# Kernel optimization log

Hardware: AMD Instinct MI355X
Metric: run time of the kernel (lower is better)

Reference implementation:

```python
import math
import jax, jax.numpy as jnp
import numpy as np

NH, HD, CHUNK, PAST, FUT = 12, 128, 128, 127, 0  # heads, head_dim, chunk, left-1, right
CTX = CHUNK + PAST + FUT                          # 255
Q_SCALE = HD ** (-0.5) / math.log(2.0)
K_SCALE = math.log1p(math.e) / math.log(2.0)
SOFTCAP = 50.0


def setup_inputs() -> dict:
    key = jax.random.key(0)
    ks = jax.random.split(key, 8)
    B, S, H = 4, 4096, NH * HD
    return {
        "hidden_states": jax.random.normal(ks[0], (B, S, H), jnp.float32),
        "position_embeddings": jax.random.normal(ks[1], (CTX, H), jnp.float32),
        "Wq": jax.random.normal(ks[2], (H, H), jnp.float32) * 0.02,
        "Wk": jax.random.normal(ks[3], (H, H), jnp.float32) * 0.02,
        "Wv": jax.random.normal(ks[4], (H, H), jnp.float32) * 0.02,
        "Wrel": jax.random.normal(ks[5], (H, H), jnp.float32) * 0.02,
        "Wpost": jax.random.normal(ks[6], (H, H), jnp.float32) * 0.02,
        "per_dim_scale": jax.random.normal(ks[7], (HD,), jnp.float32) * 0.1,
    }


def reference(hidden_states, position_embeddings, Wq, Wk, Wv, Wrel, Wpost, per_dim_scale):
    B, S, H = hidden_states.shape
    # projections -> [B, S, nh, hd]; per-dim softplus scaling on queries (Gemma audio)
    q = (hidden_states @ Wq.T).reshape(B, S, NH, HD)
    q = q * (Q_SCALE * jax.nn.softplus(per_dim_scale))
    k = (hidden_states @ Wk.T).reshape(B, S, NH, HD) * K_SCALE
    v = (hidden_states @ Wv.T).reshape(B, S, NH, HD)

    NB = (S + CHUNK - 1) // CHUNK
    pad = NB * CHUNK - S
    q_blk = jnp.pad(q, ((0, 0), (0, pad), (0, 0), (0, 0))).reshape(B, NB, CHUNK, NH, HD)

    def extract_block_context(x):
        # pad [PAST] front, [FUT + CHUNK - 1] back; overlapping windows of CTX, stride CHUNK
        xp = jnp.pad(x, ((0, 0), (PAST, FUT + CHUNK - 1), (0, 0), (0, 0)))
        idx = jnp.arange(NB)[:, None] * CHUNK + jnp.arange(CTX)[None, :]  # [NB, CTX]
        return xp[:, idx]  # [B, NB, CTX, nh, hd]

    k_ctx = extract_block_context(k)
    v_ctx = extract_block_context(v)

    # content scores: [B, nh, NB, CHUNK, CTX]
    ac = jnp.einsum('bnchd,bnxhd->bhncx', q_blk, k_ctx)

    # relative-position scores with Transformer-XL style rel_shift
    rel_k = (position_embeddings @ Wrel.T).reshape(-1, NH, HD)  # [P, nh, hd]
    bd = jnp.einsum('bnchd,phd->bhncp', q_blk, rel_k)            # [B, nh, NB, CHUNK, P]
    P = bd.shape[-1]
    bd = jnp.pad(bd, ((0, 0), (0, 0), (0, 0), (0, 0), (0, CTX + 1 - P)))
    bd = bd.reshape(B, NH, NB, CHUNK * (CTX + 1))[..., : CHUNK * CTX]
    bd = bd.reshape(B, NH, NB, CHUNK, CTX)

    logits = SOFTCAP * jnp.tanh((ac + bd) / SOFTCAP)  # softcap
    w = jax.nn.softmax(logits, axis=-1)

    out = jnp.einsum('bhncx,bnxhd->bnchd', w, v_ctx)  # [B, NB, CHUNK, nh, hd]
    out = out.reshape(B, NB * CHUNK, NH * HD)[:, :S]
    return out @ Wpost.T
```

## Files before the change

### kernel.cpp

```cpp
#include <hip/hip_runtime.h>
#include <hip/hip_bf16.h>
#include <math.h>


#define NH_    12
#define HD_    128
#define H_     1536
#define B_     4
#define S_     4096
#define CHUNK_ 128
#define CTX_   255
#define NB_CH  32
#define QKW_   3072
#define BSTR_  4352

typedef unsigned short u16;
typedef short bf16x8 __attribute__((ext_vector_type(8)));
typedef float f32x4 __attribute__((ext_vector_type(4)));

static constexpr float Q_SCALE_F = (float)(0.08838834764831845 / 0.6931471805599453);
static constexpr float K_SCALE_F = (float)(1.3132616875182228 / 0.6931471805599453);

__device__ __forceinline__ u16 f2bf(float f) {
    __hip_bfloat16 h = __float2bfloat16(f);
    return __builtin_bit_cast(u16, h);
}
__device__ __forceinline__ float bf2f(u16 u) {
    unsigned int t = ((unsigned int)u) << 16;
    return __builtin_bit_cast(float, t);
}
__device__ __forceinline__ float fast_tanh(float t) {
    float u = __expf(-2.f * fabsf(t));
    float r = (1.f - u) / (1.f + u);
    return (t < 0.f) ? -r : r;
}

__device__ __forceinline__ void gload_lds16(const u16* src_global, u16* dst_lds) {
    __builtin_amdgcn_global_load_lds(
        (const __attribute__((address_space(1))) unsigned int*)src_global,
        (__attribute__((address_space(3))) unsigned int*)dst_lds,
        16, 0, 0);
}

__global__ __launch_bounds__(256)
void conv_bf16(const float* __restrict__ src, long long base,
               u16* __restrict__ dst, long long n,
               long long zero_below, long long zero_from,
               int mode, const float* __restrict__ pds, int ncols)
{
    long long i = ((long long)blockIdx.x * 256 + threadIdx.x) * 4;
    if (i >= n) return;
    float4 v = make_float4(0.f, 0.f, 0.f, 0.f);
    if (i >= zero_below && i < zero_from)
        v = *(const float4*)(src + base + i);
    float s = 1.f;
    if (mode == 1) {
        int row = (int)(i / ncols);
        float x = pds[row & 127];
        float sp = (x > 20.f) ? x : log1pf(__expf(x));
        s = Q_SCALE_F * sp;
    } else if (mode == 2) {
        s = K_SCALE_F;
    }
    ushort4 o = make_ushort4(f2bf(v.x * s), f2bf(v.y * s), f2bf(v.z * s), f2bf(v.w * s));
    *(ushort4*)(dst + i) = o;
}

__global__ __launch_bounds__(256)
void conv_hs(const float* __restrict__ src, long long src_row0,
             u16* __restrict__ dst, long long nelem)
{
    long long i = ((long long)blockIdx.x * 256 + threadIdx.x) * 4;
    if (i >= nelem) return;
    const int row = (int)(i / H_);
    const int col = (int)(i - (long long)row * H_);
    const int b = row / BSTR_;
    const int local = row - b * BSTR_;
    float4 v = make_float4(0.f, 0.f, 0.f, 0.f);
    if (local >= 128 && local < 128 + S_) {
        const long long srow = src_row0 + (long long)b * S_ + local - 128;
        v = *(const float4*)(src + srow * H_ + col);
    }
    ushort4 o = make_ushort4(f2bf(v.x), f2bf(v.y), f2bf(v.z), f2bf(v.w));
    *(ushort4*)(dst + i) = o;
}

#define STAGE(kt, bufc) do {                                                   \
    const int _ko = (kt) << 5;                                                 \
    gload_lds16(srcA[0] + _ko, lds + (bufc) * 4096 + pbase[0]);                \
    gload_lds16(srcA[1] + _ko, lds + (bufc) * 4096 + pbase[1]);                \
    gload_lds16(srcB[0] + _ko, lds + 16384 + (bufc) * 4096 + pbase[0]);        \
    gload_lds16(srcB[1] + _ko, lds + 16384 + (bufc) * 4096 + pbase[1]);        \
} while (0)

#define READF(afX, bfX, b) do {                                                \
    _Pragma("unroll")                                                          \
    for (int m = 0; m < 4; ++m)                                                \
        afX[m] = *(const bf16x8*)&lds[(b) * 4096 + (wr + m * 16 + lr) * 32 + sw8]; \
    _Pragma("unroll")                                                          \
    for (int n = 0; n < 4; ++n)                                                \
        bfX[n] = *(const bf16x8*)&lds[16384 + (b) * 4096 + (wc + n * 16 + lr) * 32 + sw8]; \
} while (0)

#define MFMA16(afX, bfX) do {                                                  \
    __builtin_amdgcn_s_setprio(1);                                             \
    _Pragma("unroll")                                                          \
    for (int m = 0; m < 4; ++m)                                                \
        _Pragma("unroll")                                                      \
        for (int n = 0; n < 4; ++n)                                            \
            acc[m][n] = __builtin_amdgcn_mfma_f32_16x16x32_bf16(afX[m], bfX[n], acc[m][n], 0, 0, 0); \
    __builtin_amdgcn_s_setprio(0);                                             \
} while (0)

#define ITER(t, b, afC, bfC, afN, bfN) do {                                    \
    if ((t) + 2 < nk) {                                                        \
        STAGE((t) + 2, ((b) + 2) & 3);                                         \
        asm volatile("s_waitcnt vmcnt(4)" ::: "memory");                       \
    } else {                                                                   \
        asm volatile("s_waitcnt vmcnt(0)" ::: "memory");                       \
    }                                                                          \
    __builtin_amdgcn_s_barrier();                                              \
    if ((t) + 1 < nk) READF(afN, bfN, ((b) + 1) & 3);                          \
    MFMA16(afC, bfC);                                                          \
} while (0)

template<int OUTB>
__global__ __launch_bounds__(256)
void gemm_bt(const u16* __restrict__ A, const u16* __restrict__ B,
             void* __restrict__ Cp, int M, int N, int K, int ldc)
{
    __shared__ __align__(16) u16 lds[32768];

    const int tid = threadIdx.x;
    const int w = tid >> 6, l = tid & 63;
    const int lr = l & 15, lg = l >> 4;
    const int bm = blockIdx.y * 128, bn = blockIdx.x * 128;
    const int wr = (w >> 1) * 64, wc = (w & 1) * 64;

    const int sw8 = (lg ^ ((lr >> 1) & 3)) * 8;

    const u16* srcA[2];
    const u16* srcB[2];
    int pbase[2];
#pragma unroll
    for (int c = 0; c < 2; ++c) {
        const int p = (w * 2 + c) * 64 + l;
        const int row = p >> 2;
        const int s_log = (p & 3) ^ ((row >> 1) & 3);
        pbase[c] = p * 8;
        srcA[c] = A + (size_t)(bm + row) * K + s_log * 8;
        srcB[c] = B + (size_t)(bn + row) * K + s_log * 8;
    }

    f32x4 acc[4][4];
#pragma unroll
    for (int m = 0; m < 4; ++m)
#pragma unroll
        for (int n = 0; n < 4; ++n) acc[m][n] = (f32x4){0.f, 0.f, 0.f, 0.f};

    const int nk = K >> 5;
    bf16x8 af0[4], bf0[4], af1[4], bf1[4];

    STAGE(0, 0);
    STAGE(1, 1);
    asm volatile("s_waitcnt vmcnt(4)" ::: "memory");
    __builtin_amdgcn_s_barrier();
    READF(af0, bf0, 0);

    for (int t0 = 0; t0 < nk; t0 += 4) {
        ITER(t0 + 0, 0, af0, bf0, af1, bf1);
        ITER(t0 + 1, 1, af1, bf1, af0, bf0);
        ITER(t0 + 2, 2, af0, bf0, af1, bf1);
        ITER(t0 + 3, 3, af1, bf1, af0, bf0);
    }

    if (OUTB) {
#pragma unroll
        for (int h = 0; h < 2; ++h) {
            if (wr == h * 64) {
#pragma unroll
                for (int m = 0; m < 4; ++m)
#pragma unroll
                    for (int n = 0; n < 4; ++n)
#pragma unroll
                        for (int r = 0; r < 4; ++r)
                            lds[(m * 16 + lg * 4 + r) * 136 + wc + n * 16 + lr] =
                                f2bf(acc[m][n][r]);
            }
            __syncthreads();
#pragma unroll
            for (int it = 0; it < 4; ++it) {
                const int sid = it * 256 + tid;
                const int row = sid >> 4, sl = sid & 15;
                int4 val = *(const int4*)&lds[row * 136 + sl * 8];
                *(int4*)((u16*)Cp + (size_t)(bm + h * 64 + row) * ldc + bn + sl * 8) = val;
            }
            __syncthreads();
        }
    } else {
#pragma unroll
        for (int m = 0; m < 4; ++m)
#pragma unroll
            for (int n = 0; n < 4; ++n)
#pragma unroll
                for (int r = 0; r < 4; ++r) {
                    const int row = bm + wr + m * 16 + lg * 4 + r;
                    const int col = bn + wc + n * 16 + lr;
                    ((float*)Cp)[(size_t)row * ldc + col] = acc[m][n][r];
                }
    }
}

__global__ __launch_bounds__(512)
void attn_mfma(const u16* __restrict__ qk, const u16* __restrict__ vT,
               const u16* __restrict__ relk, u16* __restrict__ attn_out,
               int vld)
{
    __shared__ __align__(16) u16 kv_s[256 * 128];
    __shared__ __align__(16) u16 g_s[128 * 264];

    const int ln = blockIdx.x, h = blockIdx.y, bz = blockIdx.z;
    const int tid = threadIdx.x;
    const int w = tid >> 6, l = tid & 63;
    const int lr = l & 15, lg = l >> 4;
    const size_t qbase = (size_t)bz * BSTR_;
    const size_t qrow0 = qbase + (size_t)(ln + 1) * 128;

    bf16x8 qa[4];
    {
        const u16* qp = qk + (qrow0 + w * 16 + lr) * QKW_ + h * HD_ + lg * 8;
#pragma unroll
        for (int kk = 0; kk < 4; ++kk) qa[kk] = *(const bf16x8*)(qp + kk * 32);
    }

#pragma unroll
    for (int it = 0; it < 8; ++it) {
        const int p = it * 512 + tid;
        const int row = p >> 4;
        const int s_log = (p & 15) ^ (row & 15);
        gload_lds16(relk + (size_t)row * H_ + h * HD_ + s_log * 8, kv_s + p * 8);
    }
    __syncthreads();

    f32x4 sacc[16];
#pragma unroll
    for (int n = 0; n < 16; ++n) sacc[n] = (f32x4){0.f, 0.f, 0.f, 0.f};
#pragma unroll
    for (int n = 0; n < 16; ++n)
#pragma unroll
        for (int kk = 0; kk < 4; ++kk) {
            int row = n * 16 + lr;
            int sl = kk * 4 + lg;
            bf16x8 bfrag = *(const bf16x8*)&kv_s[row * 128 + ((sl ^ (row & 15)) << 3)];
            sacc[n] = __builtin_amdgcn_mfma_f32_16x16x32_bf16(qa[kk], bfrag, sacc[n], 0, 0, 0);
        }

    const int c = w * 16 + lg * 4;
#pragma unroll
    for (int n = 0; n < 16; ++n)
#pragma unroll
        for (int r = 0; r < 4; ++r)
            g_s[(c + r) * 264 + n * 16 + lr] = f2bf(sacc[n][r]);
    __syncthreads();

#pragma unroll
    for (int it = 0; it < 8; ++it) {
        const int p = it * 512 + tid;
        const int row = p >> 4;
        const int s_log = (p & 15) ^ (row & 15);
        gload_lds16(qk + (qbase + (size_t)(ln * 128 + 1 + row)) * QKW_ + 1536 + h * HD_ + s_log * 8,
                    kv_s + p * 8);
    }
    __syncthreads();

#pragma unroll
    for (int n = 0; n < 16; ++n) sacc[n] = (f32x4){0.f, 0.f, 0.f, 0.f};
#pragma unroll
    for (int n = 0; n < 16; ++n)
#pragma unroll
        for (int kk = 0; kk < 4; ++kk) {
            int row = n * 16 + lr;
            int sl = kk * 4 + lg;
            bf16x8 bfrag = *(const bf16x8*)&kv_s[row * 128 + ((sl ^ (row & 15)) << 3)];
            sacc[n] = __builtin_amdgcn_mfma_f32_16x16x32_bf16(qa[kk], bfrag, sacc[n], 0, 0, 0);
        }

#pragma unroll
    for (int n = 0; n < 16; ++n)
#pragma unroll
        for (int r = 0; r < 4; ++r) {
            int cc = c + r;
            int x = n * 16 + lr;
            float val;
            if (x == 255) {
                val = -1e30f;
            } else {
                int dx = x - cc;
                u16 bdu = (dx >= 0) ? g_s[cc * 264 + dx]
                                    : g_s[(cc - 1) * 264 + dx + 256];
                float t = (sacc[n][r] + bf2f(bdu)) * (1.f / 50.f);
                val = 50.f * fast_tanh(t);
            }
            sacc[n][r] = val;
        }

#pragma unroll
    for (int r = 0; r < 4; ++r) {
        float m = -1e30f;
#pragma unroll
        for (int n = 0; n < 16; ++n) m = fmaxf(m, sacc[n][r]);
#pragma unroll
        for (int off = 1; off < 16; off <<= 1) m = fmaxf(m, __shfl_xor(m, off, 16));
        float s = 0.f;
#pragma unroll
        for (int n = 0; n < 16; ++n) {
            float e = __expf(sacc[n][r] - m);
            sacc[n][r] = e;
            s += e;
        }
#pragma unroll
        for (int off = 1; off < 16; off <<= 1) s += __shfl_xor(s, off, 16);
        float inv = 1.f / s;
#pragma unroll
        for (int n = 0; n < 16; ++n) sacc[n][r] *= inv;
    }
    __syncthreads();

#pragma unroll
    for (int n = 0; n < 16; ++n)
#pragma unroll
        for (int r = 0; r < 4; ++r)
            g_s[(c + r) * 264 + n * 16 + lr] = f2bf(sacc[n][r]);

#pragma unroll
    for (int it = 0; it < 8; ++it) {
        const int p = it * 512 + tid;
        const int d = p >> 5;
        const int s_log = (p & 31) ^ (d & 15);
        gload_lds16(vT + (size_t)(h * HD_ + d) * vld + qbase + ln * 128 + 1 + s_log * 8,
                    kv_s + p * 8);
    }
    __syncthreads();

    f32x4 oacc[8];
#pragma unroll
    for (int n = 0; n < 8; ++n) oacc[n] = (f32x4){0.f, 0.f, 0.f, 0.f};
#pragma unroll
    for (int kk = 0; kk < 8; ++kk) {
        int prow = w * 16 + lr;
        bf16x8 pa = *(const bf16x8*)&g_s[prow * 264 + kk * 32 + lg * 8];
#pragma unroll
        for (int n = 0; n < 8; ++n) {
            int d = n * 16 + lr;
            int sl = kk * 4 + lg;
            bf16x8 vb = *(const bf16x8*)&kv_s[d * 256 + ((sl ^ (d & 15)) << 3)];
            oacc[n] = __builtin_amdgcn_mfma_f32_16x16x32_bf16(pa, vb, oacc[n], 0, 0, 0);
        }
    }

    __syncthreads();
#pragma unroll
    for (int n = 0; n < 8; ++n)
#pragma unroll
        for (int r = 0; r < 4; ++r)
            kv_s[(c + r) * 136 + n * 16 + lr] = f2bf(oacc[n][r]);
    __syncthreads();
#pragma unroll
    for (int it = 0; it < 4; ++it) {
        const int sid = it * 512 + tid;
        const int row = sid >> 4, sl = sid & 15;
        int4 val = *(const int4*)&kv_s[row * 136 + sl * 8];
        *(int4*)(attn_out + ((size_t)bz * S_ + (size_t)(ln * 128 + row)) * H_ + h * HD_ + sl * 8) = val;
    }
}

extern "C" void kernel_launch(void* const* d_in, const int* in_sizes, int n_in,
                              void* d_out, int out_size, void* d_ws, size_t ws_size,
                              hipStream_t stream)
{
    (void)in_sizes; (void)n_in; (void)out_size;

    const float* hs    = (const float*)d_in[0];
    const float* pos   = (const float*)d_in[1];
    const float* Wq    = (const float*)d_in[2];
    const float* Wk    = (const float*)d_in[3];
    const float* Wv    = (const float*)d_in[4];
    const float* Wrel  = (const float*)d_in[5];
    const float* Wpost = (const float*)d_in[6];
    const float* pds   = (const float*)d_in[7];
    float* out = (float*)d_out;

    const long long WW = (long long)H_ * H_;
    const long long POSN = 256LL * H_;
    const long long fixed_elems = 5 * WW + 2 * POSN;

    int NB = 0;
    const int cand[3] = {4, 2, 1};
    for (int ci = 0; ci < 3; ++ci) {
        const int nb = cand[ci];
        const long long R = (long long)nb * BSTR_;
        const long long seg = R * (H_ + QKW_ + H_) + (long long)nb * S_ * H_;
        if ((fixed_elems + seg) * 2 <= (long long)ws_size) { NB = nb; break; }
    }
    if (NB == 0) return;

    const long long R = (long long)NB * BSTR_;
    const int vld = (int)R;

    u16* wqkb   = (u16*)d_ws;
    u16* wvb    = wqkb + 2 * WW;
    u16* wpostb = wvb + WW;
    u16* wrelb  = wpostb + WW;
    u16* posb   = wrelb + WW;
    u16* relkb  = posb + POSN;
    u16* hsb    = relkb + POSN;
    u16* qkb    = hsb + R * H_;
    u16* vTb    = qkb + R * QKW_;
    u16* attb   = vTb + (long long)H_ * R;

    dim3 blk(256);
    const long long BIG = 1LL << 60;

    conv_bf16<<<dim3(WW / 1024), blk, 0, stream>>>(Wq, 0, wqkb,        WW, 0, BIG, 1, pds, H_);
    conv_bf16<<<dim3(WW / 1024), blk, 0, stream>>>(Wk, 0, wqkb + WW,   WW, 0, BIG, 2, nullptr, H_);
    conv_bf16<<<dim3(WW / 1024), blk, 0, stream>>>(Wv, 0, wvb,         WW, 0, BIG, 0, nullptr, H_);
    conv_bf16<<<dim3(WW / 1024), blk, 0, stream>>>(Wpost, 0, wpostb,   WW, 0, BIG, 0, nullptr, H_);
    conv_bf16<<<dim3(WW / 1024), blk, 0, stream>>>(Wrel, 0, wrelb,     WW, 0, BIG, 0, nullptr, H_);
    conv_bf16<<<dim3(POSN / 1024), blk, 0, stream>>>(pos, 0, posb, POSN, 0, 255LL * H_, 0, nullptr, H_);

    gemm_bt<1><<<dim3(H_ / 128, 2), blk, 0, stream>>>(posb, wrelb, relkb, 256, H_, H_, H_);

    const long long hn = R * H_;
    for (int s = 0; s < B_ / NB; ++s) {
        const long long row0 = (long long)s * NB * S_;

        conv_hs<<<dim3((unsigned)(hn / 1024)), blk, 0, stream>>>(hs, row0, hsb, hn);

        gemm_bt<1><<<dim3(QKW_ / 128, (unsigned)(R / 128)), blk, 0, stream>>>(
            hsb, wqkb, qkb, (int)R, QKW_, H_, QKW_);

        gemm_bt<1><<<dim3((unsigned)(R / 128), H_ / 128), blk, 0, stream>>>(
            wvb, hsb, vTb, H_, (int)R, H_, vld);

        attn_mfma<<<dim3(NB_CH, NH_, NB), dim3(512), 0, stream>>>(
            qkb, vTb, relkb, attb, vld);

        gemm_bt<0><<<dim3(H_ / 128, (unsigned)((long long)NB * S_ / 128)), blk, 0, stream>>>(
            attb, wpostb, out + row0 * H_, (int)(NB * S_), H_, H_, H_);
    }
}
```

Measured before the change: 609.4 us.

## Add 256x256-tile GEMM with 512 threads for the large projections

Adds a new GEMM kernel that uses 256x256 output tiles computed by 8 waves, each wave owning a 128x64 sub-tile. The QK, V and output projections now use it, while the small rel-pos GEMM keeps the old 128x128 kernel. The larger tiles raise arithmetic intensity and reuse of LDS-staged operands, cutting global loads per FLOP. In exchange they need 128 KB of LDS and more accumulator registers per thread, which lowers occupancy and gives fewer blocks for load balancing across CUs.

```diff
diff --git a/kernel.cpp b/kernel.cpp
--- a/kernel.cpp
+++ b/kernel.cpp
@@ -124,10 +124,9 @@
     MFMA16(afC, bfC);                                                          \
 } while (0)
 
-template<int OUTB>
 __global__ __launch_bounds__(256)
 void gemm_bt(const u16* __restrict__ A, const u16* __restrict__ B,
-             void* __restrict__ Cp, int M, int N, int K, int ldc)
+             u16* __restrict__ Cp, int M, int N, int K, int ldc)
 {
     __shared__ __align__(16) u16 lds[32768];
 
@@ -136,7 +135,6 @@
     const int lr = l & 15, lg = l >> 4;
     const int bm = blockIdx.y * 128, bn = blockIdx.x * 128;
     const int wr = (w >> 1) * 64, wc = (w & 1) * 64;
-
     const int sw8 = (lg ^ ((lr >> 1) & 3)) * 8;
 
     const u16* srcA[2];
@@ -174,38 +172,143 @@
         ITER(t0 + 3, 3, af1, bf1, af0, bf0);
     }
 
+#pragma unroll
+    for (int h = 0; h < 2; ++h) {
+        if (wr == h * 64) {
+#pragma unroll
+            for (int m = 0; m < 4; ++m)
+#pragma unroll
+                for (int n = 0; n < 4; ++n)
+#pragma unroll
+                    for (int r = 0; r < 4; ++r)
+                        lds[(m * 16 + lg * 4 + r) * 136 + wc + n * 16 + lr] =
+                            f2bf(acc[m][n][r]);
+        }
+        __syncthreads();
+#pragma unroll
+        for (int it = 0; it < 4; ++it) {
+            const int sid = it * 256 + tid;
+            const int row = sid >> 4, sl = sid & 15;
+            int4 val = *(const int4*)&lds[row * 136 + sl * 8];
+            *(int4*)(Cp + (size_t)(bm + h * 64 + row) * ldc + bn + sl * 8) = val;
+        }
+        __syncthreads();
+    }
+}
+
+#define STG2(kt, bufc) do {                                                    \
+    const int _ko = (kt) << 5;                                                 \
+    gload_lds16(srcA[0] + _ko, lds + (bufc) * 16384 + pbase[0]);               \
+    gload_lds16(srcA[1] + _ko, lds + (bufc) * 16384 + pbase[1]);               \
+    gload_lds16(srcB[0] + _ko, lds + (bufc) * 16384 + 8192 + pbase[0]);        \
+    gload_lds16(srcB[1] + _ko, lds + (bufc) * 16384 + 8192 + pbase[1]);        \
+} while (0)
+
+#define IT2(t, b) do {                                                         \
+    if ((t) + 2 < nk) {                                                        \
+        STG2((t) + 2, ((b) + 2) & 3);                                          \
+        asm volatile("s_waitcnt vmcnt(8)" ::: "memory");                       \
+    } else if ((t) + 2 == nk) {                                                \
+        asm volatile("s_waitcnt vmcnt(4)" ::: "memory");                       \
+    } else {                                                                   \
+        asm volatile("s_waitcnt vmcnt(0)" ::: "memory");                       \
+    }                                                                          \
+    __builtin_amdgcn_s_barrier();                                              \
+    bf16x8 af[8], bfr[4];                                                      \
+    _Pragma("unroll")                                                          \
+    for (int m = 0; m < 8; ++m)                                                \
+        af[m] = *(const bf16x8*)&lds[(b) * 16384 + (mbase + m * 16 + lr) * 32 + sw8]; \
+    _Pragma("unroll")                                                          \
+    for (int n = 0; n < 4; ++n)                                                \
+        bfr[n] = *(const bf16x8*)&lds[(b) * 16384 + 8192 + (nbase + n * 16 + lr) * 32 + sw8]; \
+    __builtin_amdgcn_s_setprio(1);                                             \
+    _Pragma("unroll")                                                          \
+    for (int m = 0; m < 8; ++m)                                                \
+        _Pragma("unroll")                                                      \
+        for (int n = 0; n < 4; ++n)                                            \
+            acc[m][n] = __builtin_amdgcn_mfma_f32_16x16x32_bf16(af[m], bfr[n], acc[m][n], 0, 0, 0); \
+    __builtin_amdgcn_s_setprio(0);                                             \
+} while (0)
+
+template<int OUTB>
+__global__ __launch_bounds__(512, 2)
+void gemm256(const u16* __restrict__ A, const u16* __restrict__ B,
+             void* __restrict__ Cp, int M, int N, int K, int ldc)
+{
+    __shared__ __align__(16) u16 lds[65536];
+
+    const int tid = threadIdx.x;
+    const int w = tid >> 6, l = tid & 63;
+    const int lr = l & 15, lg = l >> 4;
+    const int wrow = w >> 2, wcol = w & 3;
+    const int bm = blockIdx.y * 256, bn = blockIdx.x * 256;
+    const int mbase = wrow * 128;
+    const int nbase = wcol * 64;
+    const int sw8 = (lg ^ ((lr >> 1) & 3)) * 8;
+
+    const u16* srcA[2];
+    const u16* srcB[2];
+    int pbase[2];
+#pragma unroll
+    for (int c = 0; c < 2; ++c) {
+        const int p = c * 512 + tid;
+        const int row = p >> 2;
+        const int s_log = (p & 3) ^ ((row >> 1) & 3);
+        pbase[c] = p * 8;
+        srcA[c] = A + (size_t)(bm + row) * K + s_log * 8;
+        srcB[c] = B + (size_t)(bn + row) * K + s_log * 8;
+    }
+
+    f32x4 acc[8][4];
+#pragma unroll
+    for (int m = 0; m < 8; ++m)
+#pragma unroll
+        for (int n = 0; n < 4; ++n) acc[m][n] = (f32x4){0.f, 0.f, 0.f, 0.f};
+
+    const int nk = K >> 5;
+    STG2(0, 0);
+    STG2(1, 1);
+    for (int t0 = 0; t0 < nk; t0 += 4) {
+        IT2(t0 + 0, 0);
+        IT2(t0 + 1, 1);
+        IT2(t0 + 2, 2);
+        IT2(t0 + 3, 3);
+    }
+
+    __syncthreads();
+
     if (OUTB) {
 #pragma unroll
         for (int h = 0; h < 2; ++h) {
-            if (wr == h * 64) {
-#pragma unroll
-                for (int m = 0; m < 4; ++m)
+            if (wrow == h) {
+#pragma unroll
+                for (int m = 0; m < 8; ++m)
 #pragma unroll
                     for (int n = 0; n < 4; ++n)
 #pragma unroll
                         for (int r = 0; r < 4; ++r)
-                            lds[(m * 16 + lg * 4 + r) * 136 + wc + n * 16 + lr] =
+                            lds[(m * 16 + lg * 4 + r) * 264 + nbase + n * 16 + lr] =
                                 f2bf(acc[m][n][r]);
             }
             __syncthreads();
 #pragma unroll
-            for (int it = 0; it < 4; ++it) {
-                const int sid = it * 256 + tid;
-                const int row = sid >> 4, sl = sid & 15;
-                int4 val = *(const int4*)&lds[row * 136 + sl * 8];
-                *(int4*)((u16*)Cp + (size_t)(bm + h * 64 + row) * ldc + bn + sl * 8) = val;
+            for (int it = 0; it < 8; ++it) {
+                const int sid = it * 512 + tid;
+                const int row = sid >> 5, sl = sid & 31;
+                int4 val = *(const int4*)&lds[row * 264 + sl * 8];
+                *(int4*)((u16*)Cp + (size_t)(bm + h * 128 + row) * ldc + bn + sl * 8) = val;
             }
             __syncthreads();
         }
     } else {
 #pragma unroll
-        for (int m = 0; m < 4; ++m)
+        for (int m = 0; m < 8; ++m)
 #pragma unroll
             for (int n = 0; n < 4; ++n)
 #pragma unroll
                 for (int r = 0; r < 4; ++r) {
-                    const int row = bm + wr + m * 16 + lg * 4 + r;
-                    const int col = bn + wc + n * 16 + lr;
+                    const int row = bm + mbase + m * 16 + lg * 4 + r;
+                    const int col = bn + nbase + n * 16 + lr;
                     ((float*)Cp)[(size_t)row * ldc + col] = acc[m][n][r];
                 }
     }
@@ -428,7 +531,7 @@
     conv_bf16<<<dim3(WW / 1024), blk, 0, stream>>>(Wrel, 0, wrelb,     WW, 0, BIG, 0, nullptr, H_);
     conv_bf16<<<dim3(POSN / 1024), blk, 0, stream>>>(pos, 0, posb, POSN, 0, 255LL * H_, 0, nullptr, H_);
 
-    gemm_bt<1><<<dim3(H_ / 128, 2), blk, 0, stream>>>(posb, wrelb, relkb, 256, H_, H_, H_);
+    gemm_bt<<<dim3(H_ / 128, 2), blk, 0, stream>>>(posb, wrelb, relkb, 256, H_, H_, H_);
 
     const long long hn = R * H_;
     for (int s = 0; s < B_ / NB; ++s) {
@@ -436,16 +539,16 @@
 
         conv_hs<<<dim3((unsigned)(hn / 1024)), blk, 0, stream>>>(hs, row0, hsb, hn);
 
-        gemm_bt<1><<<dim3(QKW_ / 128, (unsigned)(R / 128)), blk, 0, stream>>>(
+        gemm256<1><<<dim3(QKW_ / 256, (unsigned)(R / 256)), dim3(512), 0, stream>>>(
             hsb, wqkb, qkb, (int)R, QKW_, H_, QKW_);
 
-        gemm_bt<1><<<dim3((unsigned)(R / 128), H_ / 128), blk, 0, stream>>>(
+        gemm256<1><<<dim3((unsigned)(R / 256), H_ / 256), dim3(512), 0, stream>>>(
             wvb, hsb, vTb, H_, (int)R, H_, vld);
 
         attn_mfma<<<dim3(NB_CH, NH_, NB), dim3(512), 0, stream>>>(
             qkb, vTb, relkb, attb, vld);
 
-        gemm_bt<0><<<dim3(H_ / 128, (unsigned)((long long)NB * S_ / 128)), blk, 0, stream>>>(
+        gemm256<0><<<dim3(H_ / 256, (unsigned)((long long)NB * S_ / 256)), dim3(512), 0, stream>>>(
             attb, wpostb, out + row0 * H_, (int)(NB * S_), H_, H_, H_);
     }
 }
```

After: 573.1 us. 6.0% less time.
